# Kernel tuning notes

Hardware: AMD Instinct MI355X
Metric: run time of the kernel (lower is better)

The kernel has to match this reference:

```python
import jax, jax.numpy as jnp
import numpy as np

B, T, C, H = 2, 2048, 1024, 16
HD = C // H  # head_dim = 64


def setup_inputs() -> dict:
    key = jax.random.key(0)
    k1, k2, k3 = jax.random.split(key, 3)
    x = jax.random.normal(k1, (B, T, C), dtype=jnp.float32)
    w_attn = jax.random.normal(k2, (3 * C, C), dtype=jnp.float32) * 0.02
    w_proj = jax.random.normal(k3, (C, C), dtype=jnp.float32) * 0.02
    # RoPE frequencies: theta_i = 10000^(-2i/head_dim)
    inv_freq = 1.0 / (10000.0 ** (jnp.arange(0, HD, 2, dtype=jnp.float32) / HD))  # (HD//2,)
    angles = jnp.arange(T, dtype=jnp.float32)[:, None] * inv_freq[None, :]        # (T, HD//2)
    return {
        "x": x,
        "w_attn": w_attn,
        "w_proj": w_proj,
        "freqs_cos": jnp.cos(angles),
        "freqs_sin": jnp.sin(angles),
    }


def _rope(t, cos, sin):
    # t: (B, T, H, HD); cos/sin: (T, HD//2) broadcast to (1, T, 1, HD//2)
    te = t[..., 0::2]
    to = t[..., 1::2]
    c = cos[None, :, None, :]
    s = sin[None, :, None, :]
    re = te * c - to * s
    ro = te * s + to * c
    # interleave back: (..., HD//2, 2) -> (..., HD)
    return jnp.stack([re, ro], axis=-1).reshape(t.shape)


def reference(x, w_attn, w_proj, freqs_cos, freqs_sin):
    b, t, c = x.shape
    qkv = jnp.einsum('btc,fc->btf', x, w_attn)          # (B, T, 3C)
    q, k, v = jnp.split(qkv, 3, axis=2)
    q = q.reshape(b, t, H, HD)
    k = k.reshape(b, t, H, HD)
    v = v.reshape(b, t, H, HD)
    q = _rope(q, freqs_cos, freqs_sin)
    k = _rope(k, freqs_cos, freqs_sin)
    # causal SDPA
    scale = 1.0 / np.sqrt(HD).astype(np.float32)
    scores = jnp.einsum('bqhd,bkhd->bhqk', q, k) * scale  # (B, H, T, T)
    mask = jnp.tril(jnp.ones((t, t), dtype=bool))
    scores = jnp.where(mask[None, None, :, :], scores, jnp.finfo(scores.dtype).min)
    attn = jax.nn.softmax(scores, axis=-1)
    y = jnp.einsum('bhqk,bkhd->bqhd', attn, v).reshape(b, t, c)
    return jnp.einsum('btc,oc->bto', y, w_proj)
```

## Files before the change

### kernel.cpp

```cpp
#include <hip/hip_runtime.h>
#include <math.h>

#define B_  2
#define T_  2048
#define C_  1024
#define H_  16
#define HD_ 64
#define F3_ 3072

typedef __attribute__((ext_vector_type(8))) __bf16 bf16x8;
typedef __attribute__((ext_vector_type(4))) float  f32x4;

__device__ __forceinline__ ushort f2bf(float f) {
  uint32_t u = __builtin_bit_cast(uint32_t, f);
  u += 0x7fff + ((u >> 16) & 1);
  return (ushort)(u >> 16);
}
__device__ __forceinline__ float bf2f(ushort u) {
  return __builtin_bit_cast(float, (uint32_t)u << 16);
}
__device__ __forceinline__ void gll16(void* lds, const void* g) {
  __builtin_amdgcn_global_load_lds(
      (const __attribute__((address_space(1))) void*)g,
      (__attribute__((address_space(3))) void*)lds, 16, 0, 0);
}

__global__ __launch_bounds__(256) void cvt_f32_bf16(const float* __restrict__ in,
                                                    ushort* __restrict__ out, int n4) {
  int i = blockIdx.x * 256 + threadIdx.x;
  if (i >= n4) return;
  float4 v = ((const float4*)in)[i];
  ushort4 o;
  o.x = f2bf(v.x); o.y = f2bf(v.y); o.z = f2bf(v.z); o.w = f2bf(v.w);
  ((ushort4*)out)[i] = o;
}

template<int MODE>
__global__ __launch_bounds__(256) void gemm_mfma(
    const ushort* __restrict__ A, const ushort* __restrict__ Bm,
    void* __restrict__ Cout, ushort* __restrict__ vT,
    int M, int N, int K)
{
  __shared__ ushort As[128][64];
  __shared__ ushort Bs[128][64];
  const int tid  = threadIdx.x;
  const int lane = tid & 63, w = tid >> 6;
  const int wr = w >> 1, wc = w & 1;
  const int ll = lane & 15, lg = lane >> 4;
  const int r8 = lane >> 3;
  const int gc = ((lane & 7) ^ r8) << 3;
  const int m0 = blockIdx.x * 128, n0 = blockIdx.y * 128;

  f32x4 acc[4][4] = {};

  for (int k0 = 0; k0 < K; k0 += 64) {
    __syncthreads();
#pragma unroll
    for (int iss = 0; iss < 4; ++iss) {
      int rb = w * 32 + iss * 8;
      gll16(&As[rb][0], A  + (size_t)(m0 + rb + r8) * K + k0 + gc);
      gll16(&Bs[rb][0], Bm + (size_t)(n0 + rb + r8) * K + k0 + gc);
    }
    __syncthreads();
#pragma unroll
    for (int ks = 0; ks < 2; ++ks) {
      const int sw = ((ks * 4 + lg) ^ (ll & 7)) * 8;
      bf16x8 af[4], bfr[4];
#pragma unroll
      for (int mi = 0; mi < 4; ++mi)
        af[mi] = *(const bf16x8*)&As[wr * 64 + mi * 16 + ll][sw];
#pragma unroll
      for (int ni = 0; ni < 4; ++ni)
        bfr[ni] = *(const bf16x8*)&Bs[wc * 64 + ni * 16 + ll][sw];
#pragma unroll
      for (int mi = 0; mi < 4; ++mi)
#pragma unroll
        for (int ni = 0; ni < 4; ++ni)
          acc[mi][ni] = __builtin_amdgcn_mfma_f32_16x16x32_bf16(
              af[mi], bfr[ni], acc[mi][ni], 0, 0, 0);
    }
  }

  const int mrow = wr * 64 + lg * 4;
  const int ncol = wc * 64 + ll;
  if (MODE == 0) {
    float* C = (float*)Cout;
#pragma unroll
    for (int mi = 0; mi < 4; ++mi)
#pragma unroll
      for (int ni = 0; ni < 4; ++ni)
#pragma unroll
        for (int r = 0; r < 4; ++r)
          C[(size_t)(m0 + mrow + mi * 16 + r) * N + n0 + ncol + ni * 16] =
              acc[mi][ni][r];
  } else {
    if (n0 < 2 * C_) {
      ushort* q = (ushort*)Cout;
#pragma unroll
      for (int mi = 0; mi < 4; ++mi)
#pragma unroll
        for (int ni = 0; ni < 4; ++ni)
#pragma unroll
          for (int r = 0; r < 4; ++r)
            q[(size_t)(m0 + mrow + mi * 16 + r) * F3_ + n0 + ncol + ni * 16] =
                f2bf(acc[mi][ni][r]);
    } else {
      const int bb = m0 >> 11;
      const int tb = (m0 & 2047) + mrow;
#pragma unroll
      for (int mi = 0; mi < 4; ++mi)
#pragma unroll
        for (int ni = 0; ni < 4; ++ni) {
          int f  = n0 + ncol + ni * 16 - 2 * C_;
          int hh = f >> 6, d = f & 63;
          ushort4 o;
          o.x = f2bf(acc[mi][ni][0]); o.y = f2bf(acc[mi][ni][1]);
          o.z = f2bf(acc[mi][ni][2]); o.w = f2bf(acc[mi][ni][3]);
          *(ushort4*)&vT[(((size_t)(bb * H_ + hh) * HD_ + d) << 11) + tb + mi * 16] = o;
        }
    }
  }
}

__global__ __launch_bounds__(256) void rope_bf(ushort* __restrict__ qkv,
                                               const float* __restrict__ fcos,
                                               const float* __restrict__ fsin) {
  int idx = blockIdx.x * 256 + threadIdx.x;
  int i2 = idx & 15;
  int h  = (idx >> 4) & 15;
  int t  = (idx >> 8) & 2047;
  int b  = idx >> 19;
  int fi = t * 32 + i2 * 2;
  float c0 = fcos[fi], s0 = fsin[fi], c1 = fcos[fi + 1], s1 = fsin[fi + 1];
  size_t base = (size_t)(b * T_ + t) * F3_ + h * HD_ + i2 * 4;
  ushort4 qv = *(ushort4*)&qkv[base];
  ushort4 qo;
  { float e = bf2f(qv.x), o = bf2f(qv.y);
    qo.x = f2bf((e * c0 - o * s0) * 0.125f);
    qo.y = f2bf((e * s0 + o * c0) * 0.125f); }
  { float e = bf2f(qv.z), o = bf2f(qv.w);
    qo.z = f2bf((e * c1 - o * s1) * 0.125f);
    qo.w = f2bf((e * s1 + o * c1) * 0.125f); }
  *(ushort4*)&qkv[base] = qo;
  ushort4 kv = *(ushort4*)&qkv[base + C_];
  ushort4 ko;
  { float e = bf2f(kv.x), o = bf2f(kv.y);
    ko.x = f2bf(e * c0 - o * s0);
    ko.y = f2bf(e * s0 + o * c0); }
  { float e = bf2f(kv.z), o = bf2f(kv.w);
    ko.z = f2bf(e * c1 - o * s1);
    ko.w = f2bf(e * s1 + o * c1); }
  *(ushort4*)&qkv[base + C_] = ko;
}

__global__ __launch_bounds__(256) void attn_mfma(
    const ushort* __restrict__ qkv, const ushort* __restrict__ vT,
    ushort* __restrict__ y)
{
  __shared__ ushort Qs[64][64];
  __shared__ ushort Ks[2][64][64], VTs[2][64][64];
  __shared__ ushort Ps[4][16][72];

  const int qt = 31 - blockIdx.y;
  const int bh = blockIdx.x;
  const int b = bh >> 4, h = bh & 15;
  const int q0 = qt * 64;
  const int tid = threadIdx.x, lane = tid & 63, w = tid >> 6;
  const int ll = lane & 15, lg = lane >> 4;
  const int r8 = lane >> 3;
  const int gc = ((lane & 7) ^ r8) << 3;
  const float NEG = -3.0e38f;

  const ushort* qb = qkv + (size_t)(b * T_) * F3_ + h * HD_;
  const ushort* kb = qb + C_;
  const ushort* vb = vT + ((size_t)(b * H_ + h) * HD_ << 11);

#pragma unroll
  for (int iss = 0; iss < 2; ++iss) {
    int rb = w * 16 + iss * 8;
    gll16(&Qs[rb][0], qb + (size_t)(q0 + rb + r8) * F3_ + gc);
    gll16(&Ks[0][rb][0],  kb + (size_t)(rb + r8) * F3_ + gc);
    gll16(&VTs[0][rb][0], vb + ((size_t)(rb + r8) << 11) + gc);
  }
  __syncthreads();

  bf16x8 qf[2];
#pragma unroll
  for (int ks = 0; ks < 2; ++ks)
    qf[ks] = *(const bf16x8*)&Qs[w * 16 + ll][((ks * 4 + lg) ^ (ll & 7)) * 8];

  f32x4 oacc[4] = {};
  float m_ = NEG, l_ = 0.f;
  int cur = 0;

  for (int kt = 0; kt <= qt; ++kt) {
    if (kt < qt) {
#pragma unroll
      for (int iss = 0; iss < 2; ++iss) {
        int rb = w * 16 + iss * 8;
        gll16(&Ks[cur ^ 1][rb][0],
              kb + (size_t)((kt + 1) * 64 + rb + r8) * F3_ + gc);
        gll16(&VTs[cur ^ 1][rb][0],
              vb + ((size_t)(rb + r8) << 11) + (kt + 1) * 64 + gc);
      }
    }

    f32x4 sacc[4] = {};
#pragma unroll
    for (int ks = 0; ks < 2; ++ks) {
      const int sw = ((ks * 4 + lg) ^ (ll & 7)) * 8;
      bf16x8 kf[4];
#pragma unroll
      for (int j = 0; j < 4; ++j)
        kf[j] = *(const bf16x8*)&Ks[cur][j * 16 + ll][sw];
#pragma unroll
      for (int j = 0; j < 4; ++j)
        sacc[j] = __builtin_amdgcn_mfma_f32_16x16x32_bf16(kf[j], qf[ks], sacc[j], 0, 0, 0);
    }

    if (kt == qt) {
#pragma unroll
      for (int j = 0; j < 4; ++j)
#pragma unroll
        for (int r = 0; r < 4; ++r)
          if (j * 16 + lg * 4 + r > w * 16 + ll) sacc[j][r] = NEG;
    }

    float tmax;
    {
      float t0 = fmaxf(fmaxf(sacc[0][0], sacc[0][1]), fmaxf(sacc[0][2], sacc[0][3]));
      float t1 = fmaxf(fmaxf(sacc[1][0], sacc[1][1]), fmaxf(sacc[1][2], sacc[1][3]));
      float t2 = fmaxf(fmaxf(sacc[2][0], sacc[2][1]), fmaxf(sacc[2][2], sacc[2][3]));
      float t3 = fmaxf(fmaxf(sacc[3][0], sacc[3][1]), fmaxf(sacc[3][2], sacc[3][3]));
      tmax = fmaxf(fmaxf(t0, t1), fmaxf(t2, t3));
      tmax = fmaxf(tmax, __shfl_xor(tmax, 16));
      tmax = fmaxf(tmax, __shfl_xor(tmax, 32));
    }
    if (!__all(tmax <= m_ + 8.f)) {
      float mnew = fmaxf(m_, tmax);
      float al = __expf(m_ - mnew);
      l_ *= al;
      m_ = mnew;
#pragma unroll
      for (int r = 0; r < 4; ++r) {
        float alr = __shfl(al, lg * 4 + r);
#pragma unroll
        for (int dj = 0; dj < 4; ++dj) oacc[dj][r] *= alr;
      }
    }
    float psum = 0.f;
#pragma unroll
    for (int j = 0; j < 4; ++j) {
      float p0 = __expf(sacc[j][0] - m_);
      float p1 = __expf(sacc[j][1] - m_);
      float p2 = __expf(sacc[j][2] - m_);
      float p3 = __expf(sacc[j][3] - m_);
      psum += (p0 + p1) + (p2 + p3);
      ushort4 pk;
      pk.x = f2bf(p0); pk.y = f2bf(p1); pk.z = f2bf(p2); pk.w = f2bf(p3);
      *(ushort4*)&Ps[w][ll][j * 16 + lg * 4] = pk;
    }
    psum += __shfl_xor(psum, 16);
    psum += __shfl_xor(psum, 32);
    l_ += psum;

#pragma unroll
    for (int ks = 0; ks < 2; ++ks) {
      bf16x8 pf = *(const bf16x8*)&Ps[w][ll][ks * 32 + lg * 8];
      const int sw = ((ks * 4 + lg) ^ (ll & 7)) * 8;
#pragma unroll
      for (int dj = 0; dj < 4; ++dj) {
        bf16x8 vf = *(const bf16x8*)&VTs[cur][dj * 16 + ll][sw];
        oacc[dj] = __builtin_amdgcn_mfma_f32_16x16x32_bf16(pf, vf, oacc[dj], 0, 0, 0);
      }
    }

    __syncthreads();
    cur ^= 1;
  }

#pragma unroll
  for (int r = 0; r < 4; ++r) {
    float lr = __shfl(l_, lg * 4 + r);
    float inv = 1.0f / lr;
    int row = q0 + w * 16 + lg * 4 + r;
#pragma unroll
    for (int dj = 0; dj < 4; ++dj)
      y[(size_t)(b * T_ + row) * C_ + h * HD_ + dj * 16 + ll] =
          f2bf(oacc[dj][r] * inv);
  }
}

extern "C" void kernel_launch(void* const* d_in, const int* in_sizes, int n_in,
                              void* d_out, int out_size, void* d_ws, size_t ws_size,
                              hipStream_t stream) {
  const float* x      = (const float*)d_in[0];
  const float* w_attn = (const float*)d_in[1];
  const float* w_proj = (const float*)d_in[2];
  const float* fcos   = (const float*)d_in[3];
  const float* fsin   = (const float*)d_in[4];
  float* out = (float*)d_out;

  ushort* xb   = (ushort*)d_ws;
  ushort* wab  = xb   + (size_t)4096 * 1024;
  ushort* wpb  = wab  + (size_t)3072 * 1024;
  ushort* qkvb = wpb  + (size_t)1024 * 1024;
  ushort* vt   = qkvb + (size_t)4096 * 3072;
  ushort* yb   = vt   + (size_t)32 * 64 * 2048;

  cvt_f32_bf16<<<4096, 256, 0, stream>>>(x,      xb,  1048576);
  cvt_f32_bf16<<<3072, 256, 0, stream>>>(w_attn, wab,  786432);
  cvt_f32_bf16<<<1024, 256, 0, stream>>>(w_proj, wpb,  262144);

  { dim3 g(32, 24); gemm_mfma<1><<<g, 256, 0, stream>>>(xb, wab, qkvb, vt, 4096, F3_, C_); }
  rope_bf<<<4096, 256, 0, stream>>>(qkvb, fcos, fsin);
  { dim3 g(32, 32); attn_mfma<<<g, 256, 0, stream>>>(qkvb, vt, yb); }
  { dim3 g(32, 8);  gemm_mfma<0><<<g, 256, 0, stream>>>(yb, wpb, out, nullptr, 4096, C_, C_); }
}
```

Measured before the change: 115.0 us.

## Fuse conversions, use exp2 softmax, truncate P to bf16, add MFMA priority hints

Three fp32-to-bf16 conversion launches become a single kernel over a concatenated index range. The softmax now runs in base 2: log2(e) is folded into the Q scale during RoPE, exp2 replaces expf, and the lazy-rescale threshold is adjusted to match. P values are converted to bf16 by truncation instead of round-to-nearest, which adds a small bias in exchange for fewer ALU ops. s_setprio brackets are placed around the MFMA blocks in both the GEMM and attention kernels, and V fragment loads are hoisted ahead of their MFMAs.

```diff
diff --git a/kernel.cpp b/kernel.cpp
--- a/kernel.cpp
+++ b/kernel.cpp
@@ -8,6 +8,11 @@
 #define HD_ 64
 #define F3_ 3072
 
+#define X4_   ((B_ * T_ * C_) / 4)
+#define WA4_  ((F3_ * C_) / 4)
+#define WP4_  ((C_ * C_) / 4)
+#define TOT4_ (X4_ + WA4_ + WP4_)
+
 typedef __attribute__((ext_vector_type(8))) __bf16 bf16x8;
 typedef __attribute__((ext_vector_type(4))) float  f32x4;
 
@@ -25,11 +30,18 @@
       (__attribute__((address_space(3))) void*)lds, 16, 0, 0);
 }
 
-__global__ __launch_bounds__(256) void cvt_f32_bf16(const float* __restrict__ in,
-                                                    ushort* __restrict__ out, int n4) {
+__global__ __launch_bounds__(256) void cvt_all(const float* __restrict__ x,
+                                               const float* __restrict__ wa,
+                                               const float* __restrict__ wp,
+                                               ushort* __restrict__ out) {
+  static_assert(X4_ == 1048576 && WA4_ == 786432 && WP4_ == 262144, "sizes");
+  static_assert((X4_ % 256) == 0 && ((X4_ + WA4_) % 256) == 0, "block-uniform");
   int i = blockIdx.x * 256 + threadIdx.x;
-  if (i >= n4) return;
-  float4 v = ((const float4*)in)[i];
+  const float* src; int off;
+  if (i < X4_)              { src = x;  off = i; }
+  else if (i < X4_ + WA4_)  { src = wa; off = i - X4_; }
+  else                      { src = wp; off = i - (X4_ + WA4_); }
+  float4 v = ((const float4*)src)[off];
   ushort4 o;
   o.x = f2bf(v.x); o.y = f2bf(v.y); o.z = f2bf(v.z); o.w = f2bf(v.w);
   ((ushort4*)out)[i] = o;
@@ -72,12 +84,14 @@
 #pragma unroll
       for (int ni = 0; ni < 4; ++ni)
         bfr[ni] = *(const bf16x8*)&Bs[wc * 64 + ni * 16 + ll][sw];
+      __builtin_amdgcn_s_setprio(1);
 #pragma unroll
       for (int mi = 0; mi < 4; ++mi)
 #pragma unroll
         for (int ni = 0; ni < 4; ++ni)
           acc[mi][ni] = __builtin_amdgcn_mfma_f32_16x16x32_bf16(
               af[mi], bfr[ni], acc[mi][ni], 0, 0, 0);
+      __builtin_amdgcn_s_setprio(0);
     }
   }
 
@@ -122,6 +136,7 @@
   }
 }
 
+#define QSC 0.18033688f
 __global__ __launch_bounds__(256) void rope_bf(ushort* __restrict__ qkv,
                                                const float* __restrict__ fcos,
                                                const float* __restrict__ fsin) {
@@ -136,11 +151,11 @@
   ushort4 qv = *(ushort4*)&qkv[base];
   ushort4 qo;
   { float e = bf2f(qv.x), o = bf2f(qv.y);
-    qo.x = f2bf((e * c0 - o * s0) * 0.125f);
-    qo.y = f2bf((e * s0 + o * c0) * 0.125f); }
+    qo.x = f2bf((e * c0 - o * s0) * QSC);
+    qo.y = f2bf((e * s0 + o * c0) * QSC); }
   { float e = bf2f(qv.z), o = bf2f(qv.w);
-    qo.z = f2bf((e * c1 - o * s1) * 0.125f);
-    qo.w = f2bf((e * s1 + o * c1) * 0.125f); }
+    qo.z = f2bf((e * c1 - o * s1) * QSC);
+    qo.w = f2bf((e * s1 + o * c1) * QSC); }
   *(ushort4*)&qkv[base] = qo;
   ushort4 kv = *(ushort4*)&qkv[base + C_];
   ushort4 ko;
@@ -157,9 +172,9 @@
     const ushort* __restrict__ qkv, const ushort* __restrict__ vT,
     ushort* __restrict__ y)
 {
-  __shared__ ushort Qs[64][64];
-  __shared__ ushort Ks[2][64][64], VTs[2][64][64];
-  __shared__ ushort Ps[4][16][72];
+  __shared__ __align__(16) ushort Qs[64][64];
+  __shared__ __align__(16) ushort Ks[2][64][64], VTs[2][64][64];
+  __shared__ __align__(16) ushort Ps[4][16][72];
 
   const int qt = 31 - blockIdx.y;
   const int bh = blockIdx.x;
@@ -213,9 +228,11 @@
 #pragma unroll
       for (int j = 0; j < 4; ++j)
         kf[j] = *(const bf16x8*)&Ks[cur][j * 16 + ll][sw];
+      __builtin_amdgcn_s_setprio(1);
 #pragma unroll
       for (int j = 0; j < 4; ++j)
         sacc[j] = __builtin_amdgcn_mfma_f32_16x16x32_bf16(kf[j], qf[ks], sacc[j], 0, 0, 0);
+      __builtin_amdgcn_s_setprio(0);
     }
 
     if (kt == qt) {
@@ -236,9 +253,9 @@
       tmax = fmaxf(tmax, __shfl_xor(tmax, 16));
       tmax = fmaxf(tmax, __shfl_xor(tmax, 32));
     }
-    if (!__all(tmax <= m_ + 8.f)) {
+    if (!__all(tmax <= m_ + 11.5441f)) {
       float mnew = fmaxf(m_, tmax);
-      float al = __expf(m_ - mnew);
+      float al = __builtin_amdgcn_exp2f(m_ - mnew);
       l_ *= al;
       m_ = mnew;
 #pragma unroll
@@ -251,14 +268,17 @@
     float psum = 0.f;
 #pragma unroll
     for (int j = 0; j < 4; ++j) {
-      float p0 = __expf(sacc[j][0] - m_);
-      float p1 = __expf(sacc[j][1] - m_);
-      float p2 = __expf(sacc[j][2] - m_);
-      float p3 = __expf(sacc[j][3] - m_);
+      float p0 = __builtin_amdgcn_exp2f(sacc[j][0] - m_);
+      float p1 = __builtin_amdgcn_exp2f(sacc[j][1] - m_);
+      float p2 = __builtin_amdgcn_exp2f(sacc[j][2] - m_);
+      float p3 = __builtin_amdgcn_exp2f(sacc[j][3] - m_);
       psum += (p0 + p1) + (p2 + p3);
-      ushort4 pk;
-      pk.x = f2bf(p0); pk.y = f2bf(p1); pk.z = f2bf(p2); pk.w = f2bf(p3);
-      *(ushort4*)&Ps[w][ll][j * 16 + lg * 4] = pk;
+      uint u0 = __builtin_bit_cast(uint32_t, p0) >> 16;
+      uint u1 = __builtin_bit_cast(uint32_t, p1) & 0xffff0000u;
+      uint u2 = __builtin_bit_cast(uint32_t, p2) >> 16;
+      uint u3 = __builtin_bit_cast(uint32_t, p3) & 0xffff0000u;
+      uint2 pk = make_uint2(u0 | u1, u2 | u3);
+      *(uint2*)&Ps[w][ll][j * 16 + lg * 4] = pk;
     }
     psum += __shfl_xor(psum, 16);
     psum += __shfl_xor(psum, 32);
@@ -268,11 +288,15 @@
     for (int ks = 0; ks < 2; ++ks) {
       bf16x8 pf = *(const bf16x8*)&Ps[w][ll][ks * 32 + lg * 8];
       const int sw = ((ks * 4 + lg) ^ (ll & 7)) * 8;
-#pragma unroll
-      for (int dj = 0; dj < 4; ++dj) {
-        bf16x8 vf = *(const bf16x8*)&VTs[cur][dj * 16 + ll][sw];
-        oacc[dj] = __builtin_amdgcn_mfma_f32_16x16x32_bf16(pf, vf, oacc[dj], 0, 0, 0);
-      }
+      bf16x8 vf[4];
+#pragma unroll
+      for (int dj = 0; dj < 4; ++dj)
+        vf[dj] = *(const bf16x8*)&VTs[cur][dj * 16 + ll][sw];
+      __builtin_amdgcn_s_setprio(1);
+#pragma unroll
+      for (int dj = 0; dj < 4; ++dj)
+        oacc[dj] = __builtin_amdgcn_mfma_f32_16x16x32_bf16(pf, vf[dj], oacc[dj], 0, 0, 0);
+      __builtin_amdgcn_s_setprio(0);
     }
 
     __syncthreads();
@@ -308,9 +332,7 @@
   ushort* vt   = qkvb + (size_t)4096 * 3072;
   ushort* yb   = vt   + (size_t)32 * 64 * 2048;
 
-  cvt_f32_bf16<<<4096, 256, 0, stream>>>(x,      xb,  1048576);
-  cvt_f32_bf16<<<3072, 256, 0, stream>>>(w_attn, wab,  786432);
-  cvt_f32_bf16<<<1024, 256, 0, stream>>>(w_proj, wpb,  262144);
+  cvt_all<<<TOT4_ / 256, 256, 0, stream>>>(x, w_attn, w_proj, xb);
 
   { dim3 g(32, 24); gemm_mfma<1><<<g, 256, 0, stream>>>(xb, wab, qkvb, vt, 4096, F3_, C_); }
   rope_bf<<<4096, 256, 0, stream>>>(qkvb, fcos, fsin);
```

Result: faster. 109.9 us (-4.5%).
